# Performance work log

Hardware: AMD Instinct MI355X
Metric: run time of the kernel (lower is better)

## Reference

```python
import jax, jax.numpy as jnp
import numpy as np

B, T, D, E, P = 4, 2048, 1024, 8, 1024

def setup_inputs() -> dict:
    key = jax.random.key(0)
    k1, k2, k3 = jax.random.split(key, 3)
    x = jax.random.normal(k1, (B, T, D), dtype=jnp.float32)
    gate_w = jax.random.normal(k2, (D, E), dtype=jnp.float32) * (1.0 / np.sqrt(D))
    gate_b = jnp.zeros((E,), dtype=jnp.float32)
    expert_w = jax.random.normal(k3, (E, D, P), dtype=jnp.float32) * (1.0 / np.sqrt(D))
    expert_b = jnp.zeros((E, P), dtype=jnp.float32)
    return {"x": x, "gate_w": gate_w, "gate_b": gate_b,
            "expert_w": expert_w, "expert_b": expert_b}

def reference(x, gate_w, gate_b, expert_w, expert_b):
    # gating: Dense(E) with softmax -> [B, T, E]
    gate = jax.nn.softmax(jnp.einsum('btd,de->bte', x, gate_w) + gate_b, axis=-1)
    # all experts as one batched GEMM: [B, T, E, P]
    expert_out = jnp.einsum('btd,edp->btep', x, expert_w) + expert_b
    # gate-weighted sum over experts -> [B, T, P]
    out = jnp.einsum('bte,btep->btp', gate, expert_out)
    return out
```

## Files before the change

### kernel.cpp

```cpp
#include <hip/hip_runtime.h>
#include <hip/hip_bf16.h>
#include <math.h>

#define M_TOT 8192
#define D_DIM 1024
#define E_NUM 8
#define P_DIM 1024
#define K_TOT (E_NUM * D_DIM)

typedef __attribute__((ext_vector_type(8))) short short8;
typedef __attribute__((ext_vector_type(4))) float f32x4;
typedef __attribute__((ext_vector_type(8))) unsigned short u16x8;

static __device__ __forceinline__ unsigned short f2bf(float f) {
  unsigned u = __builtin_bit_cast(unsigned, f);
  unsigned r = (u + 0x7fffu + ((u >> 16) & 1u)) >> 16;
  return (unsigned short)r;
}

__global__ __launch_bounds__(256) void gate_kernel(const float* __restrict__ x,
                                                   const float* __restrict__ gw,
                                                   const float* __restrict__ gb,
                                                   float* __restrict__ gate) {
  const int row  = blockIdx.x * 4 + (threadIdx.x >> 6);
  const int lane = threadIdx.x & 63;
  const float* xr = x + (size_t)row * D_DIM;
  float acc[E_NUM];
#pragma unroll
  for (int e = 0; e < E_NUM; ++e) acc[e] = 0.f;
#pragma unroll
  for (int it = 0; it < 16; ++it) {
    const int d = it * 64 + lane;
    const float xv = xr[d];
    const float4* g4 = reinterpret_cast<const float4*>(gw + (size_t)d * E_NUM);
    float4 a = g4[0], b = g4[1];
    acc[0] += xv * a.x; acc[1] += xv * a.y; acc[2] += xv * a.z; acc[3] += xv * a.w;
    acc[4] += xv * b.x; acc[5] += xv * b.y; acc[6] += xv * b.z; acc[7] += xv * b.w;
  }
#pragma unroll
  for (int off = 32; off >= 1; off >>= 1) {
#pragma unroll
    for (int e = 0; e < E_NUM; ++e) acc[e] += __shfl_xor(acc[e], off, 64);
  }
  if (lane == 0) {
    float v[E_NUM], mx = -1e30f;
#pragma unroll
    for (int e = 0; e < E_NUM; ++e) { v[e] = acc[e] + gb[e]; mx = fmaxf(mx, v[e]); }
    float s = 0.f;
#pragma unroll
    for (int e = 0; e < E_NUM; ++e) { v[e] = expf(v[e] - mx); s += v[e]; }
    const float inv = 1.f / s;
#pragma unroll
    for (int e = 0; e < E_NUM; ++e) gate[(size_t)row * E_NUM + e] = v[e] * inv;
  }
}


__global__ __launch_bounds__(256) void wtrans2_kernel(const float* __restrict__ w,
                                                      unsigned short* __restrict__ wt) {
  __shared__ float tile[64][65];
  const int e  = blockIdx.z;
  const int p0 = blockIdx.y * 64;
  const int d0 = blockIdx.x * 64;
  const int tx = threadIdx.x & 63;
  const int ty = threadIdx.x >> 6;
  const float* src = w + ((size_t)e * D_DIM + d0) * P_DIM + p0;
#pragma unroll
  for (int i = 0; i < 16; ++i) {
    const int dr = i * 4 + ty;
    tile[dr][tx] = src[(size_t)dr * P_DIM + tx];
  }
  __syncthreads();
#pragma unroll
  for (int i = 0; i < 16; ++i) {
    const int pr = i * 4 + ty;
    const int c = tx ^ ((pr & 7) << 3);
    wt[(size_t)(p0 + pr) * K_TOT + e * D_DIM + d0 + c] = f2bf(tile[tx][pr]);
  }
}

__global__ __launch_bounds__(256) void aprep_kernel(const float* __restrict__ x,
                                                    const float* __restrict__ gate,
                                                    unsigned short* __restrict__ ap) {
  const int tid = threadIdx.x;
  const int m   = blockIdx.x * 2 + (tid >> 7);
  const int jd  = tid & 127;
  const float4* xp = reinterpret_cast<const float4*>(x + (size_t)m * D_DIM + jd * 8);
  const float4 p = xp[0], q = xp[1];
  unsigned short* row = ap + (size_t)m * K_TOT;
  const int cbase = (jd >> 3) * 8 + ((jd & 7) ^ (m & 7));
#pragma unroll
  for (int e = 0; e < E_NUM; ++e) {
    const float gs = gate[(size_t)m * E_NUM + e];
    u16x8 v;
    v[0] = f2bf(p.x * gs); v[1] = f2bf(p.y * gs);
    v[2] = f2bf(p.z * gs); v[3] = f2bf(p.w * gs);
    v[4] = f2bf(q.x * gs); v[5] = f2bf(q.y * gs);
    v[6] = f2bf(q.z * gs); v[7] = f2bf(q.w * gs);
    *reinterpret_cast<u16x8*>(&row[(size_t)(e * 128 + cbase) * 8]) = v;
  }
}

__global__ __launch_bounds__(256, 3) void gemm_bt_kernel(
    const unsigned short* __restrict__ ap,
    const unsigned short* __restrict__ wt,
    const float* __restrict__ gate,
    const float* __restrict__ eb,
    float* __restrict__ out) {
  __shared__ unsigned short lA[128 * 64];
  __shared__ unsigned short lB[128 * 64];
  __shared__ float lG[128 * 8];
  __shared__ float lBias[E_NUM * 128];

  const int tid  = threadIdx.x;
  const int lane = tid & 63;
  const int wid  = tid >> 6;
  const int wr   = wid >> 1, wc = wid & 1;

  const int bid = blockIdx.x;
  const int swz = (bid & 7) * 64 + (bid >> 3);
  const int m0  = (swz >> 3) * 128;
  const int n0  = (swz & 7) * 128;

  reinterpret_cast<float4*>(lG)[tid] =
      reinterpret_cast<const float4*>(gate + (size_t)m0 * E_NUM)[tid];
  {
    const int e = tid >> 5, c = (tid & 31) * 4;
    *reinterpret_cast<float4*>(&lBias[e * 128 + c]) =
        *reinterpret_cast<const float4*>(&eb[(size_t)e * P_DIM + n0 + c]);
  }

  f32x4 acc[4][4];
#pragma unroll
  for (int i = 0; i < 4; ++i)
#pragma unroll
    for (int j = 0; j < 4; ++j)
#pragma unroll
      for (int k = 0; k < 4; ++k) acc[i][j][k] = 0.f;

  const int r0 = tid >> 3;
  const int c8 = tid & 7;
  const unsigned short* pA = ap + (size_t)(m0 + r0) * K_TOT + c8 * 8;
  const unsigned short* pB = wt + (size_t)(n0 + r0) * K_TOT + c8 * 8;

  for (int kt = 0; kt < K_TOT / 64; ++kt) {
    __syncthreads();
#pragma unroll
    for (int i = 0; i < 4; ++i) {
      __builtin_amdgcn_global_load_lds(
          (const __attribute__((address_space(1))) void*)(pA + (size_t)i * 32 * K_TOT),
          (__attribute__((address_space(3))) void*)&lA[(tid + i * 256) * 8], 16, 0, 0);
    }
#pragma unroll
    for (int i = 0; i < 4; ++i) {
      __builtin_amdgcn_global_load_lds(
          (const __attribute__((address_space(1))) void*)(pB + (size_t)i * 32 * K_TOT),
          (__attribute__((address_space(3))) void*)&lB[(tid + i * 256) * 8], 16, 0, 0);
    }
    __syncthreads();
#pragma unroll
    for (int kk = 0; kk < 2; ++kk) {
      const int e0 = kk * 32 + (lane >> 4) * 8;
      short8 a[4], b[4];
#pragma unroll
      for (int m = 0; m < 4; ++m) {
        const int r = wr * 64 + m * 16 + (lane & 15);
        a[m] = *reinterpret_cast<const short8*>(&lA[r * 64 + (e0 ^ ((r & 7) << 3))]);
      }
#pragma unroll
      for (int n = 0; n < 4; ++n) {
        const int r = wc * 64 + n * 16 + (lane & 15);
        b[n] = *reinterpret_cast<const short8*>(&lB[r * 64 + (e0 ^ ((r & 7) << 3))]);
      }
#pragma unroll
      for (int m = 0; m < 4; ++m)
#pragma unroll
        for (int n = 0; n < 4; ++n)
          acc[m][n] = __builtin_amdgcn_mfma_f32_16x16x32_bf16(a[m], b[n], acc[m][n], 0, 0, 0);
    }
    pA += 64;
    pB += 64;
  }

#pragma unroll
  for (int m = 0; m < 4; ++m) {
#pragma unroll
    for (int n = 0; n < 4; ++n) {
      const int rbase = wr * 64 + m * 16 + ((lane >> 4) * 4);
      const int cl    = wc * 64 + n * 16 + (lane & 15);
#pragma unroll
      for (int reg = 0; reg < 4; ++reg) {
        const int r = rbase + reg;
        float bsum = 0.f;
#pragma unroll
        for (int e = 0; e < E_NUM; ++e) bsum += lG[r * 8 + e] * lBias[e * 128 + cl];
        out[(size_t)(m0 + r) * P_DIM + n0 + cl] = acc[m][n][reg] + bsum;
      }
    }
  }
}


__global__ __launch_bounds__(256) void wtrans_kernel(const float* __restrict__ w,
                                                     unsigned short* __restrict__ wt) {
  __shared__ float tile[64][65];
  const int e  = blockIdx.z;
  const int p0 = blockIdx.y * 64;
  const int d0 = blockIdx.x * 64;
  const int tx = threadIdx.x & 63;
  const int ty = threadIdx.x >> 6;
  const float* src = w + ((size_t)e * D_DIM + d0) * P_DIM + p0;
#pragma unroll
  for (int i = 0; i < 16; ++i) {
    const int dr = i * 4 + ty;
    tile[dr][tx] = src[(size_t)dr * P_DIM + tx];
  }
  __syncthreads();
  unsigned short* dst = wt + ((size_t)e * P_DIM + p0) * D_DIM + d0;
#pragma unroll
  for (int i = 0; i < 16; ++i) {
    const int pr = i * 4 + ty;
    const int c = tx ^ ((pr & 7) << 3);
    dst[(size_t)pr * D_DIM + c] = f2bf(tile[tx][pr]);
  }
}

__global__ __launch_bounds__(256, 2) void moe_gemm_kernel(
    const float* __restrict__ x,
    const unsigned short* __restrict__ wt,
    const float* __restrict__ gate,
    const float* __restrict__ eb,
    float* __restrict__ out) {
  __shared__ unsigned short lA[128 * 64];
  __shared__ unsigned short lB[128 * 64];
  __shared__ float lG[128 * 8];
  __shared__ float lBias[E_NUM * 128];

  const int tid  = threadIdx.x;
  const int lane = tid & 63;
  const int wid  = tid >> 6;
  const int wr   = wid >> 1, wc = wid & 1;
  const int m0   = blockIdx.x * 128;
  const int n0   = blockIdx.y * 128;

  reinterpret_cast<float4*>(lG)[tid] =
      reinterpret_cast<const float4*>(gate + (size_t)m0 * E_NUM)[tid];
  {
    const int e = tid >> 5, c = (tid & 31) * 4;
    *reinterpret_cast<float4*>(&lBias[e * 128 + c]) =
        *reinterpret_cast<const float4*>(&eb[(size_t)e * P_DIM + n0 + c]);
  }
  __syncthreads();

  const int rA   = tid >> 1;
  const int colA = (tid & 1) * 32;
  const float* xrow = x + (size_t)(m0 + rA) * D_DIM + colA;

  f32x4 acc[4][4];
#pragma unroll
  for (int i = 0; i < 4; ++i)
#pragma unroll
    for (int j = 0; j < 4; ++j)
#pragma unroll
      for (int k = 0; k < 4; ++k) acc[i][j][k] = 0.f;

  for (int e = 0; e < E_NUM; ++e) {
    const float gs = lG[rA * 8 + e];
    const unsigned short* wte = wt + ((size_t)e * P_DIM + n0) * D_DIM;
    for (int kt = 0; kt < 16; ++kt) {
      __syncthreads();
      const float4* apv = reinterpret_cast<const float4*>(xrow + kt * 64);
#pragma unroll
      for (int j = 0; j < 4; ++j) {
        float4 p = apv[2 * j], q = apv[2 * j + 1];
        u16x8 v;
        v[0] = f2bf(p.x * gs); v[1] = f2bf(p.y * gs);
        v[2] = f2bf(p.z * gs); v[3] = f2bf(p.w * gs);
        v[4] = f2bf(q.x * gs); v[5] = f2bf(q.y * gs);
        v[6] = f2bf(q.z * gs); v[7] = f2bf(q.w * gs);
        const int idx = rA * 64 + ((colA + j * 8) ^ ((rA & 7) << 3));
        *reinterpret_cast<u16x8*>(&lA[idx]) = v;
      }
#pragma unroll
      for (int i = 0; i < 4; ++i) {
        const int u  = tid + i * 256;
        const int rr = u >> 3;
        const int cc = u & 7;
        const unsigned short* src = wte + (size_t)rr * D_DIM + kt * 64 + cc * 8;
        __builtin_amdgcn_global_load_lds(
            (const __attribute__((address_space(1))) void*)src,
            (__attribute__((address_space(3))) void*)&lB[u * 8], 16, 0, 0);
      }
      __syncthreads();
#pragma unroll
      for (int kk = 0; kk < 2; ++kk) {
        const int e0 = kk * 32 + (lane >> 4) * 8;
        short8 a[4], b[4];
#pragma unroll
        for (int m = 0; m < 4; ++m) {
          const int r = wr * 64 + m * 16 + (lane & 15);
          a[m] = *reinterpret_cast<const short8*>(&lA[r * 64 + (e0 ^ ((r & 7) << 3))]);
        }
#pragma unroll
        for (int n = 0; n < 4; ++n) {
          const int r = wc * 64 + n * 16 + (lane & 15);
          b[n] = *reinterpret_cast<const short8*>(&lB[r * 64 + (e0 ^ ((r & 7) << 3))]);
        }
#pragma unroll
        for (int m = 0; m < 4; ++m)
#pragma unroll
          for (int n = 0; n < 4; ++n)
            acc[m][n] = __builtin_amdgcn_mfma_f32_16x16x32_bf16(a[m], b[n], acc[m][n], 0, 0, 0);
      }
    }
  }

#pragma unroll
  for (int m = 0; m < 4; ++m) {
#pragma unroll
    for (int n = 0; n < 4; ++n) {
      const int rbase = wr * 64 + m * 16 + ((lane >> 4) * 4);
      const int cl    = wc * 64 + n * 16 + (lane & 15);
#pragma unroll
      for (int reg = 0; reg < 4; ++reg) {
        const int r = rbase + reg;
        float bsum = 0.f;
#pragma unroll
        for (int e = 0; e < E_NUM; ++e) bsum += lG[r * 8 + e] * lBias[e * 128 + cl];
        out[(size_t)(m0 + r) * P_DIM + n0 + cl] = acc[m][n][reg] + bsum;
      }
    }
  }
}


extern "C" void kernel_launch(void* const* d_in, const int* in_sizes, int n_in,
                              void* d_out, int out_size, void* d_ws, size_t ws_size,
                              hipStream_t stream) {
  const float* x  = (const float*)d_in[0];
  const float* gw = (const float*)d_in[1];
  const float* gb = (const float*)d_in[2];
  const float* ew = (const float*)d_in[3];
  const float* eb = (const float*)d_in[4];
  float* out = (float*)d_out;

  char* ws = (char*)d_ws;
  float* gate        = (float*)ws;
  unsigned short* wt = (unsigned short*)(ws + 262144);

  const size_t need_big = 262144ull + 16777216ull + 134217728ull;

  gate_kernel<<<M_TOT / 4, 256, 0, stream>>>(x, gw, gb, gate);

  if (ws_size >= need_big) {
    unsigned short* apb = (unsigned short*)(ws + 262144 + 16777216);
    wtrans2_kernel<<<dim3(D_DIM / 64, P_DIM / 64, E_NUM), 256, 0, stream>>>(ew, wt);
    aprep_kernel<<<M_TOT / 2, 256, 0, stream>>>(x, gate, apb);
    gemm_bt_kernel<<<(M_TOT / 128) * (P_DIM / 128), 256, 0, stream>>>(apb, wt, gate, eb, out);
  } else {
    wtrans_kernel<<<dim3(D_DIM / 64, P_DIM / 64, E_NUM), 256, 0, stream>>>(ew, wt);
    moe_gemm_kernel<<<dim3(M_TOT / 128, P_DIM / 128), 256, 0, stream>>>(x, wt, gate, eb, out);
  }
}
```

Before: 195.4 us.

## Triple-buffer GEMM LDS loads with 128x256 tiles and 512-thread blocks

Replaces the single-buffered 128x128 GEMM, which stalled on a barrier around every k-tile load, with a triple-buffered pipeline that prefetches two tiles ahead using partial vmcnt waits. Tiles grow to 128x256 with 8 waves per block and 256 blocks, a block-to-XCD mapping meant to improve L2 reuse, and MFMA priority hints. The bias is read from global memory in the epilogue instead of being staged in LDS. This uses more LDS (about 150 KB) and runs only one block per CU, so latency hiding rests on the pipeline rather than occupancy.

```diff
diff --git a/kernel.cpp b/kernel.cpp
--- a/kernel.cpp
+++ b/kernel.cpp
@@ -7,6 +7,7 @@
 #define E_NUM 8
 #define P_DIM 1024
 #define K_TOT (E_NUM * D_DIM)
+#define NT    (K_TOT / 64)
 
 typedef __attribute__((ext_vector_type(8))) short short8;
 typedef __attribute__((ext_vector_type(4))) float f32x4;
@@ -54,7 +55,6 @@
     for (int e = 0; e < E_NUM; ++e) gate[(size_t)row * E_NUM + e] = v[e] * inv;
   }
 }
-
 
 __global__ __launch_bounds__(256) void wtrans2_kernel(const float* __restrict__ w,
                                                       unsigned short* __restrict__ wt) {
@@ -101,34 +101,53 @@
   }
 }
 
-__global__ __launch_bounds__(256, 3) void gemm_bt_kernel(
+static __device__ __forceinline__ short8 ldfrag(const unsigned short* buf, int row, int e0) {
+  return *reinterpret_cast<const short8*>(&buf[row * 64 + (e0 ^ ((row & 7) << 3))]);
+}
+
+__global__ __launch_bounds__(512, 1) void gemm_tb_kernel(
     const unsigned short* __restrict__ ap,
     const unsigned short* __restrict__ wt,
     const float* __restrict__ gate,
     const float* __restrict__ eb,
     float* __restrict__ out) {
-  __shared__ unsigned short lA[128 * 64];
-  __shared__ unsigned short lB[128 * 64];
+  __shared__ __align__(16) unsigned short lA[3 * 128 * 64];
+  __shared__ __align__(16) unsigned short lB[3 * 256 * 64];
   __shared__ float lG[128 * 8];
-  __shared__ float lBias[E_NUM * 128];
 
   const int tid  = threadIdx.x;
   const int lane = tid & 63;
   const int wid  = tid >> 6;
-  const int wr   = wid >> 1, wc = wid & 1;
+  const int wm   = wid >> 2;
+  const int wn   = wid & 3;
+  const int l15  = lane & 15;
+  const int exb  = (lane >> 4) * 8;
 
   const int bid = blockIdx.x;
-  const int swz = (bid & 7) * 64 + (bid >> 3);
-  const int m0  = (swz >> 3) * 128;
-  const int n0  = (swz & 7) * 128;
-
-  reinterpret_cast<float4*>(lG)[tid] =
-      reinterpret_cast<const float4*>(gate + (size_t)m0 * E_NUM)[tid];
-  {
-    const int e = tid >> 5, c = (tid & 31) * 4;
-    *reinterpret_cast<float4*>(&lBias[e * 128 + c]) =
-        *reinterpret_cast<const float4*>(&eb[(size_t)e * P_DIM + n0 + c]);
-  }
+  const int xcd = bid & 7, idx = bid >> 3;
+  const int m0  = ((xcd & 1) * 32 + idx) * 128;
+  const int n0  = (xcd >> 1) * 256;
+
+  if (tid < 256)
+    reinterpret_cast<float4*>(lG)[tid] =
+        reinterpret_cast<const float4*>(gate + (size_t)m0 * E_NUM)[tid];
+
+  const unsigned short* apRow = ap + (size_t)(m0 + (tid >> 3)) * K_TOT + (tid & 7) * 8;
+  const unsigned short* wtRow = wt + (size_t)(n0 + (tid >> 3)) * K_TOT + (tid & 7) * 8;
+
+  auto stage = [&](int t, unsigned short* bA, unsigned short* bB) {
+    const int w = t & (NT - 1);
+#pragma unroll
+    for (int h = 0; h < 2; ++h)
+      __builtin_amdgcn_global_load_lds(
+          (const __attribute__((address_space(1))) void*)(apRow + (size_t)h * 64 * K_TOT + w * 64),
+          (__attribute__((address_space(3))) void*)(bA + h * 4096 + tid * 8), 16, 0, 0);
+#pragma unroll
+    for (int r = 0; r < 4; ++r)
+      __builtin_amdgcn_global_load_lds(
+          (const __attribute__((address_space(1))) void*)(wtRow + (size_t)r * 64 * K_TOT + w * 64),
+          (__attribute__((address_space(3))) void*)(bB + r * 4096 + tid * 8), 16, 0, 0);
+  };
 
   f32x4 acc[4][4];
 #pragma unroll
@@ -138,63 +157,68 @@
 #pragma unroll
       for (int k = 0; k < 4; ++k) acc[i][j][k] = 0.f;
 
-  const int r0 = tid >> 3;
-  const int c8 = tid & 7;
-  const unsigned short* pA = ap + (size_t)(m0 + r0) * K_TOT + c8 * 8;
-  const unsigned short* pB = wt + (size_t)(n0 + r0) * K_TOT + c8 * 8;
-
-  for (int kt = 0; kt < K_TOT / 64; ++kt) {
-    __syncthreads();
-#pragma unroll
-    for (int i = 0; i < 4; ++i) {
-      __builtin_amdgcn_global_load_lds(
-          (const __attribute__((address_space(1))) void*)(pA + (size_t)i * 32 * K_TOT),
-          (__attribute__((address_space(3))) void*)&lA[(tid + i * 256) * 8], 16, 0, 0);
+  stage(0, lA, lB);
+  stage(1, lA + 8192, lB + 16384);
+  asm volatile("s_waitcnt vmcnt(6)" ::: "memory");
+  __builtin_amdgcn_s_barrier();
+  asm volatile("" ::: "memory");
+
+  int cur = 0, sb = 2;
+#pragma unroll 1
+  for (int t = 0; t < NT; ++t) {
+    const unsigned short* bufA = lA + cur * 8192;
+    const unsigned short* bufB = lB + cur * 16384;
+
+    stage(t + 2, lA + sb * 8192, lB + sb * 16384);
+
+#pragma unroll
+    for (int mh = 0; mh < 2; ++mh) {
+#pragma unroll
+      for (int nh = 0; nh < 2; ++nh) {
+        const int ra0 = wm * 64 + mh * 32 + l15, ra1 = ra0 + 16;
+        const int rb0 = wn * 64 + nh * 32 + l15, rb1 = rb0 + 16;
+        short8 a00 = ldfrag(bufA, ra0, exb),      a10 = ldfrag(bufA, ra1, exb);
+        short8 b00 = ldfrag(bufB, rb0, exb),      b10 = ldfrag(bufB, rb1, exb);
+        short8 a01 = ldfrag(bufA, ra0, 32 + exb), a11 = ldfrag(bufA, ra1, 32 + exb);
+        short8 b01 = ldfrag(bufB, rb0, 32 + exb), b11 = ldfrag(bufB, rb1, 32 + exb);
+        f32x4* am0 = &acc[mh * 2][nh * 2];
+        f32x4* am1 = &acc[mh * 2 + 1][nh * 2];
+        __builtin_amdgcn_s_setprio(1);
+        am0[0] = __builtin_amdgcn_mfma_f32_16x16x32_bf16(a00, b00, am0[0], 0, 0, 0);
+        am0[1] = __builtin_amdgcn_mfma_f32_16x16x32_bf16(a00, b10, am0[1], 0, 0, 0);
+        am1[0] = __builtin_amdgcn_mfma_f32_16x16x32_bf16(a10, b00, am1[0], 0, 0, 0);
+        am1[1] = __builtin_amdgcn_mfma_f32_16x16x32_bf16(a10, b10, am1[1], 0, 0, 0);
+        am0[0] = __builtin_amdgcn_mfma_f32_16x16x32_bf16(a01, b01, am0[0], 0, 0, 0);
+        am0[1] = __builtin_amdgcn_mfma_f32_16x16x32_bf16(a01, b11, am0[1], 0, 0, 0);
+        am1[0] = __builtin_amdgcn_mfma_f32_16x16x32_bf16(a11, b01, am1[0], 0, 0, 0);
+        am1[1] = __builtin_amdgcn_mfma_f32_16x16x32_bf16(a11, b11, am1[1], 0, 0, 0);
+        __builtin_amdgcn_s_setprio(0);
+      }
     }
-#pragma unroll
-    for (int i = 0; i < 4; ++i) {
-      __builtin_amdgcn_global_load_lds(
-          (const __attribute__((address_space(1))) void*)(pB + (size_t)i * 32 * K_TOT),
-          (__attribute__((address_space(3))) void*)&lB[(tid + i * 256) * 8], 16, 0, 0);
-    }
-    __syncthreads();
-#pragma unroll
-    for (int kk = 0; kk < 2; ++kk) {
-      const int e0 = kk * 32 + (lane >> 4) * 8;
-      short8 a[4], b[4];
-#pragma unroll
-      for (int m = 0; m < 4; ++m) {
-        const int r = wr * 64 + m * 16 + (lane & 15);
-        a[m] = *reinterpret_cast<const short8*>(&lA[r * 64 + (e0 ^ ((r & 7) << 3))]);
-      }
-#pragma unroll
-      for (int n = 0; n < 4; ++n) {
-        const int r = wc * 64 + n * 16 + (lane & 15);
-        b[n] = *reinterpret_cast<const short8*>(&lB[r * 64 + (e0 ^ ((r & 7) << 3))]);
-      }
-#pragma unroll
-      for (int m = 0; m < 4; ++m)
-#pragma unroll
-        for (int n = 0; n < 4; ++n)
-          acc[m][n] = __builtin_amdgcn_mfma_f32_16x16x32_bf16(a[m], b[n], acc[m][n], 0, 0, 0);
-    }
-    pA += 64;
-    pB += 64;
-  }
-
-#pragma unroll
-  for (int m = 0; m < 4; ++m) {
-#pragma unroll
-    for (int n = 0; n < 4; ++n) {
-      const int rbase = wr * 64 + m * 16 + ((lane >> 4) * 4);
-      const int cl    = wc * 64 + n * 16 + (lane & 15);
+
+    asm volatile("s_waitcnt vmcnt(6)" ::: "memory");
+    __builtin_amdgcn_s_barrier();
+    asm volatile("" ::: "memory");
+
+    cur = (cur == 2) ? 0 : cur + 1;
+    sb  = (sb == 2) ? 0 : sb + 1;
+  }
+
+#pragma unroll
+  for (int n = 0; n < 4; ++n) {
+    const int cl = wn * 64 + n * 16 + l15;
+    float lb[E_NUM];
+#pragma unroll
+    for (int e = 0; e < E_NUM; ++e) lb[e] = eb[(size_t)e * P_DIM + n0 + cl];
+#pragma unroll
+    for (int m = 0; m < 4; ++m) {
 #pragma unroll
       for (int reg = 0; reg < 4; ++reg) {
-        const int r = rbase + reg;
-        float bsum = 0.f;
-#pragma unroll
-        for (int e = 0; e < E_NUM; ++e) bsum += lG[r * 8 + e] * lBias[e * 128 + cl];
-        out[(size_t)(m0 + r) * P_DIM + n0 + cl] = acc[m][n][reg] + bsum;
+        const int r = wm * 64 + m * 16 + (lane >> 4) * 4 + reg;
+        float bs = 0.f;
+#pragma unroll
+        for (int e = 0; e < E_NUM; ++e) bs += lG[r * 8 + e] * lb[e];
+        out[(size_t)(m0 + r) * P_DIM + n0 + cl] = acc[m][n][reg] + bs;
       }
     }
   }
@@ -356,7 +380,7 @@
     unsigned short* apb = (unsigned short*)(ws + 262144 + 16777216);
     wtrans2_kernel<<<dim3(D_DIM / 64, P_DIM / 64, E_NUM), 256, 0, stream>>>(ew, wt);
     aprep_kernel<<<M_TOT / 2, 256, 0, stream>>>(x, gate, apb);
-    gemm_bt_kernel<<<(M_TOT / 128) * (P_DIM / 128), 256, 0, stream>>>(apb, wt, gate, eb, out);
+    gemm_tb_kernel<<<256, 512, 0, stream>>>(apb, wt, gate, eb, out);
   } else {
     wtrans_kernel<<<dim3(D_DIM / 64, P_DIM / 64, E_NUM), 256, 0, stream>>>(ew, wt);
     moe_gemm_kernel<<<dim3(M_TOT / 128, P_DIM / 128), 256, 0, stream>>>(x, wt, gate, eb, out);
```

Measured after the change: 329.0 us. 1.68x slower.

## Split GEMM K dimension in two with atomic accumulation into zeroed output

Applied to the files above, without the earlier changes.

The bf16 GEMM kernel now splits the concatenated expert K dimension into two halves, doubling the block count to 1024. Each block accumulates half of K and adds its tile into the output with atomicAdd, and only the first half adds the gated bias. The output is zeroed with a memset beforehand. This aims to fill more compute units and improve occupancy, at the cost of atomic read-modify-write traffic on the output and an extra memset. The block-to-tile mapping is also reworked to group M tiles per XCD.

```diff
diff --git a/kernel.cpp b/kernel.cpp
--- a/kernel.cpp
+++ b/kernel.cpp
@@ -54,7 +54,6 @@
     for (int e = 0; e < E_NUM; ++e) gate[(size_t)row * E_NUM + e] = v[e] * inv;
   }
 }
-
 
 __global__ __launch_bounds__(256) void wtrans2_kernel(const float* __restrict__ w,
                                                       unsigned short* __restrict__ wt) {
@@ -101,7 +100,7 @@
   }
 }
 
-__global__ __launch_bounds__(256, 3) void gemm_bt_kernel(
+__global__ __launch_bounds__(256, 3) void gemm_sk2_kernel(
     const unsigned short* __restrict__ ap,
     const unsigned short* __restrict__ wt,
     const float* __restrict__ gate,
@@ -118,9 +117,11 @@
   const int wr   = wid >> 1, wc = wid & 1;
 
   const int bid = blockIdx.x;
-  const int swz = (bid & 7) * 64 + (bid >> 3);
-  const int m0  = (swz >> 3) * 128;
-  const int n0  = (swz & 7) * 128;
+  const int xcd = bid & 7, idx = bid >> 3;
+  const int kh  = idx & 1;
+  const int nt  = (idx >> 1) & 7;
+  const int mt  = xcd * 8 + (idx >> 4);
+  const int m0  = mt * 128, n0 = nt * 128;
 
   reinterpret_cast<float4*>(lG)[tid] =
       reinterpret_cast<const float4*>(gate + (size_t)m0 * E_NUM)[tid];
@@ -140,10 +141,10 @@
 
   const int r0 = tid >> 3;
   const int c8 = tid & 7;
-  const unsigned short* pA = ap + (size_t)(m0 + r0) * K_TOT + c8 * 8;
-  const unsigned short* pB = wt + (size_t)(n0 + r0) * K_TOT + c8 * 8;
-
-  for (int kt = 0; kt < K_TOT / 64; ++kt) {
+  const unsigned short* pA = ap + (size_t)(m0 + r0) * K_TOT + (size_t)kh * 4096 + c8 * 8;
+  const unsigned short* pB = wt + (size_t)(n0 + r0) * K_TOT + (size_t)kh * 4096 + c8 * 8;
+
+  for (int kt = 0; kt < 64; ++kt) {
     __syncthreads();
 #pragma unroll
     for (int i = 0; i < 4; ++i) {
@@ -191,10 +192,14 @@
 #pragma unroll
       for (int reg = 0; reg < 4; ++reg) {
         const int r = rbase + reg;
-        float bsum = 0.f;
-#pragma unroll
-        for (int e = 0; e < E_NUM; ++e) bsum += lG[r * 8 + e] * lBias[e * 128 + cl];
-        out[(size_t)(m0 + r) * P_DIM + n0 + cl] = acc[m][n][reg] + bsum;
+        float v = acc[m][n][reg];
+        if (kh == 0) {
+          float bsum = 0.f;
+#pragma unroll
+          for (int e = 0; e < E_NUM; ++e) bsum += lG[r * 8 + e] * lBias[e * 128 + cl];
+          v += bsum;
+        }
+        atomicAdd(&out[(size_t)(m0 + r) * P_DIM + n0 + cl], v);
       }
     }
   }
@@ -220,8 +225,8 @@
 #pragma unroll
   for (int i = 0; i < 16; ++i) {
     const int pr = i * 4 + ty;
-    const int c = tx ^ ((pr & 7) << 3);
-    dst[(size_t)pr * D_DIM + c] = f2bf(tile[tx][pr]);
+    const int cc = tx ^ ((pr & 7) << 3);
+    dst[(size_t)pr * D_DIM + cc] = f2bf(tile[tx][pr]);
   }
 }
 
@@ -246,9 +251,9 @@
   reinterpret_cast<float4*>(lG)[tid] =
       reinterpret_cast<const float4*>(gate + (size_t)m0 * E_NUM)[tid];
   {
-    const int e = tid >> 5, c = (tid & 31) * 4;
-    *reinterpret_cast<float4*>(&lBias[e * 128 + c]) =
-        *reinterpret_cast<const float4*>(&eb[(size_t)e * P_DIM + n0 + c]);
+    const int e = tid >> 5, cc = (tid & 31) * 4;
+    *reinterpret_cast<float4*>(&lBias[e * 128 + cc]) =
+        *reinterpret_cast<const float4*>(&eb[(size_t)e * P_DIM + n0 + cc]);
   }
   __syncthreads();
 
@@ -260,9 +265,9 @@
 #pragma unroll
   for (int i = 0; i < 4; ++i)
 #pragma unroll
-    for (int j = 0; j < 4; ++j)
-#pragma unroll
-      for (int k = 0; k < 4; ++k) acc[i][j][k] = 0.f;
+    for (int jj = 0; jj < 4; ++jj)
+#pragma unroll
+      for (int k = 0; k < 4; ++k) acc[i][jj][k] = 0.f;
 
   for (int e = 0; e < E_NUM; ++e) {
     const float gs = lG[rA * 8 + e];
@@ -271,14 +276,14 @@
       __syncthreads();
       const float4* apv = reinterpret_cast<const float4*>(xrow + kt * 64);
 #pragma unroll
-      for (int j = 0; j < 4; ++j) {
-        float4 p = apv[2 * j], q = apv[2 * j + 1];
+      for (int jj = 0; jj < 4; ++jj) {
+        float4 p = apv[2 * jj], q = apv[2 * jj + 1];
         u16x8 v;
         v[0] = f2bf(p.x * gs); v[1] = f2bf(p.y * gs);
         v[2] = f2bf(p.z * gs); v[3] = f2bf(p.w * gs);
         v[4] = f2bf(q.x * gs); v[5] = f2bf(q.y * gs);
         v[6] = f2bf(q.z * gs); v[7] = f2bf(q.w * gs);
-        const int idx = rA * 64 + ((colA + j * 8) ^ ((rA & 7) << 3));
+        const int idx = rA * 64 + ((colA + jj * 8) ^ ((rA & 7) << 3));
         *reinterpret_cast<u16x8*>(&lA[idx]) = v;
       }
 #pragma unroll
@@ -354,9 +359,10 @@
 
   if (ws_size >= need_big) {
     unsigned short* apb = (unsigned short*)(ws + 262144 + 16777216);
+    hipMemsetAsync(d_out, 0, (size_t)out_size * sizeof(float), stream);
     wtrans2_kernel<<<dim3(D_DIM / 64, P_DIM / 64, E_NUM), 256, 0, stream>>>(ew, wt);
     aprep_kernel<<<M_TOT / 2, 256, 0, stream>>>(x, gate, apb);
-    gemm_bt_kernel<<<(M_TOT / 128) * (P_DIM / 128), 256, 0, stream>>>(apb, wt, gate, eb, out);
+    gemm_sk2_kernel<<<1024, 256, 0, stream>>>(apb, wt, gate, eb, out);
   } else {
     wtrans_kernel<<<dim3(D_DIM / 64, P_DIM / 64, E_NUM), 256, 0, stream>>>(ew, wt);
     moe_gemm_kernel<<<dim3(M_TOT / 128, P_DIM / 128), 256, 0, stream>>>(x, wt, gate, eb, out);
```

Measured after the change: 202.4 us. 1.04x slower.
